# Kernel optimization log

Hardware: AMD Instinct MI355X
Metric: run time of the kernel (lower is better)

## Reference

```python
import jax, jax.numpy as jnp
import numpy as np
import math

NUM_POSE_FEAT = 64  # -> pos emb dim 128
N_NBR = 16
TEMP = 10000.0


def pos2posemb2d(pos, num_pos_feats=NUM_POSE_FEAT):
    # PETR-style 2D sine embedding; pos: (..., 2) in [0,1)
    scale = 2.0 * math.pi
    pos = pos * scale
    dim_t = jnp.arange(num_pos_feats, dtype=pos.dtype)
    dim_t = TEMP ** (2.0 * jnp.floor(dim_t / 2.0) / num_pos_feats)
    pos_x = pos[..., 0:1] / dim_t  # (..., P)
    pos_y = pos[..., 1:2] / dim_t

    def interleave(p):
        return jnp.stack([jnp.sin(p[..., 0::2]), jnp.cos(p[..., 1::2])], axis=-1).reshape(p.shape[:-1] + (-1,))

    return jnp.concatenate([interleave(pos_y), interleave(pos_x)], axis=-1)  # (..., 2P)


def mlp(x, W1, b1, W2, b2):
    return jax.nn.relu(x @ W1 + b1) @ W2 + b2


def setup_inputs() -> dict:
    key = jax.random.key(0)
    ks = jax.random.split(key, 12)
    B, S, L, D, P2 = 4, 4096, 8192, 256, 2 * NUM_POSE_FEAT
    s1 = 1.0 / np.sqrt(P2)
    s2 = 1.0 / np.sqrt(D)
    return {
        "memory": jax.random.normal(ks[0], (B, L, D), jnp.float32),
        "mem_coor": jax.random.uniform(ks[1], (B, L, 2), dtype=jnp.float32),
        "q_coor": jax.random.uniform(ks[2], (B, S, 2), dtype=jnp.float32),
        "Wq1": jax.random.normal(ks[3], (P2, D), jnp.float32) * s1,
        "bq1": jnp.zeros((D,), jnp.float32),
        "Wq2": jax.random.normal(ks[4], (D, D), jnp.float32) * s2,
        "bq2": jnp.zeros((D,), jnp.float32),
        "Wk1": jax.random.normal(ks[5], (P2, D), jnp.float32) * s1,
        "bk1": jnp.zeros((D,), jnp.float32),
        "Wk2": jax.random.normal(ks[6], (D, D), jnp.float32) * s2,
        "bk2": jnp.zeros((D,), jnp.float32),
        "B": 4,
    }


def reference(memory, mem_coor, q_coor, Wq1, bq1, Wq2, bq2, Wk1, bk1, Wk2, bk2, B):
    # memory: (B, L, D); mem_coor: (B, L, 2); q_coor: (B, S, 2)
    Bn, L, D = memory.shape
    query = mlp(pos2posemb2d(q_coor), Wq1, bq1, Wq2, bq2)      # (B, S, D) query = query_pos
    mem_pos = mlp(pos2posemb2d(mem_coor), Wk1, bk1, Wk2, bk2)  # (B, L, D)
    kv_pe = mem_pos + memory                                   # (B, L, D)

    # squared pairwise distances via matmul expansion (monotonic in true distance,
    # only the top-k ORDER is consumed downstream)
    q2 = jnp.sum(q_coor * q_coor, axis=-1)                     # (B, S)
    m2 = jnp.sum(mem_coor * mem_coor, axis=-1)                 # (B, L)
    d2 = q2[:, :, None] + m2[:, None, :] - 2.0 * jnp.einsum("bsc,blc->bsl", q_coor, mem_coor)
    _, idx = jax.lax.top_k(-d2, N_NBR)                         # (B, S, k) nearest-neighbor indices

    bidx = jnp.arange(Bn)[:, None, None]
    kv_m = kv_pe[bidx, idx]                                    # (B, S, k, D) gathered pos-embedded memory
    prod = query[:, :, None, :] * kv_m / jnp.sqrt(jnp.asarray(D, query.dtype))
    attn = jax.nn.softmax(prod, axis=-1)                       # softmax over feature dim D
    out = attn * memory[bidx, idx]                             # (B, S, k, D)
    return out
```

## Files before the change

kernel.cpp:

```cpp
#include <hip/hip_runtime.h>
#include <math.h>

#define NB 4
#define NS 4096
#define NL 8192
#define ND 256
#define NP2 128
#define NK 16

#define GCELLS 32
#define GH 0.03125f
#define CAP 256
#define EPSM 2e-5f

__device__ __forceinline__ float sum_sq_np(float x, float y) {
#pragma clang fp contract(off)
  return x * x + y * y;
}

__device__ __forceinline__ float dist2_fast(float q2, float m2, float qx, float qy,
                                            float mx, float my) {
#pragma clang fp contract(off)
  float dot = __builtin_fmaf(qy, my, qx * mx);
  float s = q2 + m2;
  return __builtin_fmaf(-2.0f, dot, s);
}

__device__ __forceinline__ unsigned f32ord(float f) {
  unsigned u = __float_as_uint(f);
  return u ^ ((unsigned)((int)u >> 31) | 0x80000000u);
}

template <int NR>
__device__ __forceinline__ unsigned extract16(const unsigned long long* candrow,
                                              int cnt, int lane,
                                              int* __restrict__ outp) {
  unsigned long long myc[NR];
#pragma unroll
  for (int j = 0; j < NR; ++j) {
    int p = lane + j * 64;
    myc[j] = (p < cnt) ? candrow[p] : ~0ull;
  }
  unsigned tau_ord = 0xffffffffu;
#pragma unroll 1
  for (int r = 0; r < NK; ++r) {
    unsigned long long m = myc[0];
#pragma unroll
    for (int j = 1; j < NR; ++j) m = myc[j] < m ? myc[j] : m;
#pragma unroll
    for (int o = 1; o < 64; o <<= 1) {
      unsigned long long other = __shfl_xor(m, o, 64);
      if (other < m) m = other;
    }
    if (lane == 0) outp[r] = (int)(unsigned)(m & 0xffffffffull);
    if (r == NK - 1) tau_ord = (unsigned)(m >> 32);
#pragma unroll
    for (int j = 0; j < NR; ++j)
      if (myc[j] == m) myc[j] = ~0ull;
  }
  return tau_ord;
}

#define RPAD 20
#define NSBLK (NB * NS / 16)

struct __align__(16) MlpSmem {
  union {
    float pe[NP2][RPAD];
    float h[ND][RPAD];
  };
};

__device__ __forceinline__ void fma16(float* acc, float wt, const float4& p0,
                                      const float4& p1, const float4& p2,
                                      const float4& p3) {
  acc[0] = fmaf(p0.x, wt, acc[0]);   acc[1] = fmaf(p0.y, wt, acc[1]);
  acc[2] = fmaf(p0.z, wt, acc[2]);   acc[3] = fmaf(p0.w, wt, acc[3]);
  acc[4] = fmaf(p1.x, wt, acc[4]);   acc[5] = fmaf(p1.y, wt, acc[5]);
  acc[6] = fmaf(p1.z, wt, acc[6]);   acc[7] = fmaf(p1.w, wt, acc[7]);
  acc[8] = fmaf(p2.x, wt, acc[8]);   acc[9] = fmaf(p2.y, wt, acc[9]);
  acc[10] = fmaf(p2.z, wt, acc[10]); acc[11] = fmaf(p2.w, wt, acc[11]);
  acc[12] = fmaf(p3.x, wt, acc[12]); acc[13] = fmaf(p3.y, wt, acc[13]);
  acc[14] = fmaf(p3.z, wt, acc[14]); acc[15] = fmaf(p3.w, wt, acc[15]);
}

__device__ __forceinline__ void loadW8(const float* __restrict__ W, int k0,
                                       int tid, float* w0, float* w1) {
#pragma unroll
  for (int u = 0; u < 8; ++u) {
    w0[u] = W[(size_t)(k0 + u) * ND + tid];
    w1[u] = W[(size_t)(k0 + u) * ND + 128 + tid];
  }
}

__device__ __forceinline__ void consume8(const float (*L)[RPAD], int k0,
                                         const float* w0, const float* w1,
                                         float* acc0, float* acc1) {
#pragma unroll
  for (int u = 0; u < 8; ++u) {
    int k = k0 + u;
    float4 p0 = *(const float4*)&L[k][0];
    float4 p1 = *(const float4*)&L[k][4];
    float4 p2 = *(const float4*)&L[k][8];
    float4 p3 = *(const float4*)&L[k][12];
    fma16(acc0, w0[u], p0, p1, p2, p3);
    fma16(acc1, w1[u], p0, p1, p2, p3);
  }
}

__global__ __launch_bounds__(128) void mlp_fused_kernel(
    const float* __restrict__ q_coor, const float* __restrict__ mem_coor,
    const float* __restrict__ memory,
    const float* __restrict__ Wq1, const float* __restrict__ bq1,
    const float* __restrict__ Wq2, const float* __restrict__ bq2,
    const float* __restrict__ Wk1, const float* __restrict__ bk1,
    const float* __restrict__ Wk2, const float* __restrict__ bk2,
    float* __restrict__ query, float* __restrict__ kv_pe) {
  __shared__ MlpSmem sm;
  const int tid = threadIdx.x;
  const int bid = blockIdx.x;
  const bool isS = bid < NSBLK;
  const float* coor = isS ? q_coor : mem_coor;
  const float* W1 = isS ? Wq1 : Wk1;
  const float* b1 = isS ? bq1 : bk1;
  const float* W2 = isS ? Wq2 : Wk2;
  const float* b2 = isS ? bq2 : bk2;
  const float* addmem = isS ? (const float*)nullptr : memory;
  float* out = isS ? query : kv_pe;
  const int row0 = (isS ? bid : bid - NSBLK) * 16;

#pragma unroll
  for (int it = 0; it < 8; ++it) {
    int e = tid + it * 128;
    int r = e >> 6;
    int rem = e & 63;
    int part = rem >> 5;
    int j = rem & 31;
    float c = coor[(size_t)(row0 + r) * 2 + (part ^ 1)];
    float inv_t = exp2f((float)j * -0.4152410118609718f);
    float arg = c * 6.2831853071795864f * inv_t;
    float sv, cv;
    sincosf(arg, &sv, &cv);
    int k0 = part * 64 + 2 * j;
    sm.pe[k0][r] = sv;
    sm.pe[k0 + 1][r] = cv;
  }
  __syncthreads();

  float acc0[16], acc1[16];
  float wA0[8], wA1[8], wB0[8], wB1[8];
  {
    float bb0 = b1[tid], bb1 = b1[tid + 128];
#pragma unroll
    for (int r = 0; r < 16; ++r) { acc0[r] = bb0; acc1[r] = bb1; }
  }
  loadW8(W1, 0, tid, wA0, wA1);
#pragma unroll 1
  for (int k0 = 0; k0 < NP2; k0 += 16) {
    loadW8(W1, k0 + 8, tid, wB0, wB1);
    consume8(sm.pe, k0, wA0, wA1, acc0, acc1);
    if (k0 + 16 < NP2) loadW8(W1, k0 + 16, tid, wA0, wA1);
    consume8(sm.pe, k0 + 8, wB0, wB1, acc0, acc1);
  }
  __syncthreads();
#pragma unroll
  for (int r = 0; r < 16; ++r) {
    sm.h[tid][r] = fmaxf(acc0[r], 0.0f);
    sm.h[tid + 128][r] = fmaxf(acc1[r], 0.0f);
  }
  __syncthreads();

  {
    float bb0 = b2[tid], bb1 = b2[tid + 128];
#pragma unroll
    for (int r = 0; r < 16; ++r) { acc0[r] = bb0; acc1[r] = bb1; }
  }
  loadW8(W2, 0, tid, wA0, wA1);
#pragma unroll 1
  for (int k0 = 0; k0 < ND; k0 += 16) {
    loadW8(W2, k0 + 8, tid, wB0, wB1);
    consume8(sm.h, k0, wA0, wA1, acc0, acc1);
    if (k0 + 16 < ND) loadW8(W2, k0 + 16, tid, wA0, wA1);
    consume8(sm.h, k0 + 8, wB0, wB1, acc0, acc1);
  }
#pragma unroll
  for (int r = 0; r < 16; ++r) {
    size_t g = (size_t)(row0 + r);
    float v0 = acc0[r], v1 = acc1[r];
    if (addmem) {
      v0 += addmem[g * ND + tid];
      v1 += addmem[g * ND + 128 + tid];
    }
    out[g * ND + tid] = v0;
    out[g * ND + 128 + tid] = v1;
  }
}

__global__ __launch_bounds__(1024) void build_kernel(
    const float* __restrict__ mem_coor, const float* __restrict__ q_coor,
    float4* __restrict__ sorted, int* __restrict__ starts,
    int* __restrict__ qord) {
  __shared__ int hist[GCELLS * GCELLS];
  __shared__ int cur[GCELLS * GCELLS];
  const int bid = blockIdx.x;
  const bool isMem = bid < NB;
  const int b = isMem ? bid : bid - NB;
  const int n = isMem ? NL : NS;
  const float2* cc = (const float2*)(isMem ? mem_coor : q_coor) + (size_t)b * n;
  const int tid = threadIdx.x;

  hist[tid] = 0;
  __syncthreads();
  for (int it = 0; it < n / 1024; ++it) {
    float2 c = cc[it * 1024 + tid];
    int cx = (int)(c.x * 32.0f); cx = cx > 31 ? 31 : cx;
    int cy = (int)(c.y * 32.0f); cy = cy > 31 ? 31 : cy;
    atomicAdd(&hist[cy * GCELLS + cx], 1);
  }
  __syncthreads();
  const int own = hist[tid];
  for (int o = 1; o < 1024; o <<= 1) {
    int v = (tid >= o) ? hist[tid - o] : 0;
    __syncthreads();
    hist[tid] += v;
    __syncthreads();
  }
  const int excl = hist[tid] - own;
  if (isMem) {
    starts[b * (GCELLS * GCELLS + 1) + tid] = excl;
    if (tid == 0) starts[b * (GCELLS * GCELLS + 1) + GCELLS * GCELLS] = NL;
  }
  cur[tid] = excl;
  __syncthreads();
  for (int it = 0; it < n / 1024; ++it) {
    int i = it * 1024 + tid;
    float2 c = cc[i];
    int cx = (int)(c.x * 32.0f); cx = cx > 31 ? 31 : cx;
    int cy = (int)(c.y * 32.0f); cy = cy > 31 ? 31 : cy;
    int pos = atomicAdd(&cur[cy * GCELLS + cx], 1);
    if (isMem) {
      sorted[(size_t)b * NL + pos] =
          make_float4(c.x, c.y, sum_sq_np(c.x, c.y), __int_as_float(i));
    } else {
      qord[b * NS + pos] = i;
    }
  }
}

__global__ __launch_bounds__(256) void topk_kernel(
    const float* __restrict__ q_coor, const float4* __restrict__ sorted,
    const int* __restrict__ starts, int* __restrict__ idx_out) {
  __shared__ unsigned long long cand[4][CAP];
  __shared__ int fcnt[4];

  const int tid = threadIdx.x;
  const int wv = tid >> 6;
  const int lane = tid & 63;
  const int qi = blockIdx.x * 4 + wv;
  const int b = qi >> 12;

  const float qx = q_coor[(size_t)qi * 2 + 0];
  const float qy = q_coor[(size_t)qi * 2 + 1];
  const float q2 = sum_sq_np(qx, qy);
  const float4* sp = sorted + (size_t)b * NL;
  const int* st = starts + b * (GCELLS * GCELLS + 1);
  int* outp = idx_out + (size_t)qi * NK;

  int ci = (int)(qx * 32.0f); ci = ci > 31 ? 31 : ci;
  int cj = (int)(qy * 32.0f); cj = cj > 31 ? 31 : cj;

  int x0 = ci - 1 < 0 ? 0 : ci - 1, x1 = ci + 1 > 31 ? 31 : ci + 1;
  int y0 = cj - 1 < 0 ? 0 : cj - 1, y1 = cj + 1 > 31 ? 31 : cj + 1;
  int cnt = 0;
  bool ovf = false;

  auto span = [&](int y, int xa, int xb) {
    int s0 = st[y * GCELLS + xa];
    int e0 = st[y * GCELLS + xb + 1];
    int len = e0 - s0;
    if (cnt + len > CAP) { ovf = true; return; }
    for (int i = lane; i < len; i += 64) {
      float4 rx = sp[s0 + i];
      float d2 = dist2_fast(q2, rx.z, qx, qy, rx.x, rx.y);
      cand[wv][cnt + i] = ((unsigned long long)f32ord(d2) << 32) |
                          (unsigned)__float_as_int(rx.w);
    }
    cnt += len;
  };

  for (int y = y0; y <= y1 && !ovf; ++y) span(y, x0, x1);

  int R = 1;
  while (!ovf) {
    unsigned tau_ord;
    if (cnt <= 128) tau_ord = extract16<2>(cand[wv], cnt, lane, outp);
    else            tau_ord = extract16<4>(cand[wv], cnt, lane, outp);
    float dxl = x0 > 0  ? qx - (float)x0 * GH        : 1e30f;
    float dxr = x1 < 31 ? (float)(x1 + 1) * GH - qx  : 1e30f;
    float dyl = y0 > 0  ? qy - (float)y0 * GH        : 1e30f;
    float dyr = y1 < 31 ? (float)(y1 + 1) * GH - qy  : 1e30f;
    float dmin = fminf(fminf(dxl, dxr), fminf(dyl, dyr));
    float bound = dmin * dmin - EPSM;
    if (cnt >= NK && tau_ord < f32ord(bound)) return;
    if (x0 == 0 && x1 == 31 && y0 == 0 && y1 == 31) return;
    ++R;
    int nx0 = ci - R < 0 ? 0 : ci - R, nx1 = ci + R > 31 ? 31 : ci + R;
    int ny0 = cj - R < 0 ? 0 : cj - R, ny1 = cj + R > 31 ? 31 : cj + R;
    if (ny0 < y0) span(ny0, nx0, nx1);
    if (ny1 > y1 && !ovf) span(ny1, nx0, nx1);
    for (int y = y0; y <= y1 && !ovf; ++y) {
      if (nx0 < x0) span(y, nx0, x0 - 1);
      if (nx1 > x1 && !ovf) span(y, x1 + 1, nx1);
    }
    x0 = nx0; x1 = nx1; y0 = ny0; y1 = ny1;
  }

  float lmin = __builtin_inff();
#pragma unroll 8
  for (int it = 0; it < NL / 64; ++it) {
    float4 rx = sp[it * 64 + lane];
    float d2 = dist2_fast(q2, rx.z, qx, qy, rx.x, rx.y);
    lmin = fminf(lmin, d2);
  }
  float tau;
  {
    float curm = lmin;
    for (int r = 0; r < NK; ++r) {
      float m = curm;
#pragma unroll
      for (int o = 1; o < 64; o <<= 1) m = fminf(m, __shfl_xor(m, o, 64));
      tau = m;
      if (curm == m) curm = __builtin_inff();
    }
  }
  if (lane == 0) fcnt[wv] = 0;
#pragma unroll 4
  for (int it = 0; it < NL / 64; ++it) {
    float4 rx = sp[it * 64 + lane];
    float d2 = dist2_fast(q2, rx.z, qx, qy, rx.x, rx.y);
    bool hit = (d2 <= tau);
    unsigned long long mask = __ballot(hit);
    if (mask) {
      int base = fcnt[wv];
      if (hit) {
        int pos = base + (int)__popcll(mask & ((1ull << lane) - 1ull));
        if (pos < CAP) {
          cand[wv][pos] = ((unsigned long long)f32ord(d2) << 32) |
                          (unsigned)__float_as_int(rx.w);
        }
      }
      if (lane == 0) fcnt[wv] = base + (int)__popcll(mask);
    }
  }
  int N = fcnt[wv];
  if (N > CAP) N = CAP;
  extract16<4>(cand[wv], N, lane, outp);
}

__global__ __launch_bounds__(256) void attn_kernel(
    const float* __restrict__ query, const float* __restrict__ kv_pe,
    const float* __restrict__ memory, const int* __restrict__ idx,
    const int* __restrict__ qord, float* __restrict__ out) {
  const int tid = threadIdx.x;
  const int wv = tid >> 6;
  const int lane = tid & 63;
  const int bid = ((blockIdx.x & 7) * (NB * NS / 4 / 8)) + (blockIdx.x >> 3);
  const int qpos = bid * 4 + wv;
  const int b = qpos >> 12;
  const int qi = b * NS + qord[qpos];

  float4 q4 = *(const float4*)(query + (size_t)qi * ND + lane * 4);
  int lv = 0;
  if (lane < NK) lv = idx[(size_t)qi * NK + lane];

#pragma unroll 4
  for (int k = 0; k < NK; ++k) {
    int l = __shfl(lv, k, 64);
    size_t base = ((size_t)b * NL + l) * ND + (size_t)lane * 4;
    float4 kv = *(const float4*)(kv_pe + base);
    float4 mm = *(const float4*)(memory + base);
    float p0 = q4.x * kv.x * 0.0625f;
    float p1 = q4.y * kv.y * 0.0625f;
    float p2 = q4.z * kv.z * 0.0625f;
    float p3 = q4.w * kv.w * 0.0625f;
    float mx = fmaxf(fmaxf(p0, p1), fmaxf(p2, p3));
#pragma unroll
    for (int o = 1; o < 64; o <<= 1) mx = fmaxf(mx, __shfl_xor(mx, o, 64));
    float e0 = expf(p0 - mx);
    float e1 = expf(p1 - mx);
    float e2 = expf(p2 - mx);
    float e3 = expf(p3 - mx);
    float s = (e0 + e1) + (e2 + e3);
#pragma unroll
    for (int o = 1; o < 64; o <<= 1) s += __shfl_xor(s, o, 64);
    float inv = 1.0f / s;
    float4 o4;
    o4.x = e0 * inv * mm.x;
    o4.y = e1 * inv * mm.y;
    o4.z = e2 * inv * mm.z;
    o4.w = e3 * inv * mm.w;
    *(float4*)(out + ((size_t)qi * NK + k) * ND + (size_t)lane * 4) = o4;
  }
}

extern "C" void kernel_launch(void* const* d_in, const int* in_sizes, int n_in,
                              void* d_out, int out_size, void* d_ws, size_t ws_size,
                              hipStream_t stream) {
  (void)in_sizes; (void)n_in; (void)out_size; (void)ws_size;
  const float* memory   = (const float*)d_in[0];
  const float* mem_coor = (const float*)d_in[1];
  const float* q_coor   = (const float*)d_in[2];
  const float* Wq1 = (const float*)d_in[3];
  const float* bq1 = (const float*)d_in[4];
  const float* Wq2 = (const float*)d_in[5];
  const float* bq2 = (const float*)d_in[6];
  const float* Wk1 = (const float*)d_in[7];
  const float* bk1 = (const float*)d_in[8];
  const float* Wk2 = (const float*)d_in[9];
  const float* bk2 = (const float*)d_in[10];

  float* query = (float*)d_ws;
  float* kv_pe = query + (size_t)NB * NS * ND;
  int*   nidx  = (int*)(kv_pe + (size_t)NB * NL * ND);
  int*   qord  = nidx + (size_t)NB * NS * NK;
  float* outp  = (float*)d_out;

  float4* sorted  = (float4*)d_out;
  int*    gstarts = (int*)((char*)d_out + (size_t)NB * NL * 16);

  hipLaunchKernelGGL(build_kernel, dim3(2 * NB), dim3(1024), 0, stream,
                     mem_coor, q_coor, sorted, gstarts, qord);
  hipLaunchKernelGGL(mlp_fused_kernel, dim3(NSBLK + NB * NL / 16), dim3(128),
                     0, stream, q_coor, mem_coor, memory,
                     Wq1, bq1, Wq2, bq2, Wk1, bk1, Wk2, bk2, query, kv_pe);
  hipLaunchKernelGGL(topk_kernel, dim3(NB * NS / 4), dim3(256), 0, stream,
                     q_coor, sorted, gstarts, nidx);
  hipLaunchKernelGGL(attn_kernel, dim3(NB * NS / 4), dim3(256), 0, stream,
                     query, kv_pe, memory, nidx, qord, outp);
}
```

Baseline: 541.8 us.

## Fuse MLP and top-k kernels into one interleaved horizontal launch

Merges the independent MLP positional-embedding kernel and the grid-based top-k neighbor search into a single launch. Blocks are interleaved in groups of 11 (3 MLP blocks, 8 top-k blocks), so compute-heavy MLP work and latency-bound search run concurrently on the CUs. Top-k blocks shrink from 4 to 2 waves to match the 128-thread block size, and shared memory becomes a union of both layouts. The cost is that occupancy and register use are now set by whichever path is heavier, which can reduce occupancy for the lighter path.

```diff
diff --git a/kernel.cpp b/kernel.cpp
--- a/kernel.cpp
+++ b/kernel.cpp
@@ -63,11 +63,25 @@
 
 #define RPAD 20
 #define NSBLK (NB * NS / 16)
+#define NMLPBLK (NSBLK + NB * NL / 16)
+#define NTKBLK (NB * NS / 2)
 
 struct __align__(16) MlpSmem {
   union {
     float pe[NP2][RPAD];
     float h[ND][RPAD];
+  };
+};
+
+struct __align__(16) TopkSmem {
+  unsigned long long cand[2][CAP];
+  int fcnt[2];
+};
+
+struct __align__(16) FusedSmem {
+  union {
+    MlpSmem mlp;
+    TopkSmem tk;
   };
 };
 
@@ -108,7 +122,8 @@
   }
 }
 
-__global__ __launch_bounds__(128) void mlp_fused_kernel(
+__device__ __forceinline__ void mlp_block(
+    int bid, int tid, MlpSmem& sm,
     const float* __restrict__ q_coor, const float* __restrict__ mem_coor,
     const float* __restrict__ memory,
     const float* __restrict__ Wq1, const float* __restrict__ bq1,
@@ -116,9 +131,6 @@
     const float* __restrict__ Wk1, const float* __restrict__ bk1,
     const float* __restrict__ Wk2, const float* __restrict__ bk2,
     float* __restrict__ query, float* __restrict__ kv_pe) {
-  __shared__ MlpSmem sm;
-  const int tid = threadIdx.x;
-  const int bid = blockIdx.x;
   const bool isS = bid < NSBLK;
   const float* coor = isS ? q_coor : mem_coor;
   const float* W1 = isS ? Wq1 : Wk1;
@@ -196,67 +208,13 @@
   }
 }
 
-__global__ __launch_bounds__(1024) void build_kernel(
-    const float* __restrict__ mem_coor, const float* __restrict__ q_coor,
-    float4* __restrict__ sorted, int* __restrict__ starts,
-    int* __restrict__ qord) {
-  __shared__ int hist[GCELLS * GCELLS];
-  __shared__ int cur[GCELLS * GCELLS];
-  const int bid = blockIdx.x;
-  const bool isMem = bid < NB;
-  const int b = isMem ? bid : bid - NB;
-  const int n = isMem ? NL : NS;
-  const float2* cc = (const float2*)(isMem ? mem_coor : q_coor) + (size_t)b * n;
-  const int tid = threadIdx.x;
-
-  hist[tid] = 0;
-  __syncthreads();
-  for (int it = 0; it < n / 1024; ++it) {
-    float2 c = cc[it * 1024 + tid];
-    int cx = (int)(c.x * 32.0f); cx = cx > 31 ? 31 : cx;
-    int cy = (int)(c.y * 32.0f); cy = cy > 31 ? 31 : cy;
-    atomicAdd(&hist[cy * GCELLS + cx], 1);
-  }
-  __syncthreads();
-  const int own = hist[tid];
-  for (int o = 1; o < 1024; o <<= 1) {
-    int v = (tid >= o) ? hist[tid - o] : 0;
-    __syncthreads();
-    hist[tid] += v;
-    __syncthreads();
-  }
-  const int excl = hist[tid] - own;
-  if (isMem) {
-    starts[b * (GCELLS * GCELLS + 1) + tid] = excl;
-    if (tid == 0) starts[b * (GCELLS * GCELLS + 1) + GCELLS * GCELLS] = NL;
-  }
-  cur[tid] = excl;
-  __syncthreads();
-  for (int it = 0; it < n / 1024; ++it) {
-    int i = it * 1024 + tid;
-    float2 c = cc[i];
-    int cx = (int)(c.x * 32.0f); cx = cx > 31 ? 31 : cx;
-    int cy = (int)(c.y * 32.0f); cy = cy > 31 ? 31 : cy;
-    int pos = atomicAdd(&cur[cy * GCELLS + cx], 1);
-    if (isMem) {
-      sorted[(size_t)b * NL + pos] =
-          make_float4(c.x, c.y, sum_sq_np(c.x, c.y), __int_as_float(i));
-    } else {
-      qord[b * NS + pos] = i;
-    }
-  }
-}
-
-__global__ __launch_bounds__(256) void topk_kernel(
+__device__ __forceinline__ void topk_block(
+    int tbid, int tid, TopkSmem& sm,
     const float* __restrict__ q_coor, const float4* __restrict__ sorted,
     const int* __restrict__ starts, int* __restrict__ idx_out) {
-  __shared__ unsigned long long cand[4][CAP];
-  __shared__ int fcnt[4];
-
-  const int tid = threadIdx.x;
   const int wv = tid >> 6;
   const int lane = tid & 63;
-  const int qi = blockIdx.x * 4 + wv;
+  const int qi = tbid * 2 + wv;
   const int b = qi >> 12;
 
   const float qx = q_coor[(size_t)qi * 2 + 0];
@@ -265,6 +223,7 @@
   const float4* sp = sorted + (size_t)b * NL;
   const int* st = starts + b * (GCELLS * GCELLS + 1);
   int* outp = idx_out + (size_t)qi * NK;
+  unsigned long long* crow = sm.cand[wv];
 
   int ci = (int)(qx * 32.0f); ci = ci > 31 ? 31 : ci;
   int cj = (int)(qy * 32.0f); cj = cj > 31 ? 31 : cj;
@@ -282,8 +241,8 @@
     for (int i = lane; i < len; i += 64) {
       float4 rx = sp[s0 + i];
       float d2 = dist2_fast(q2, rx.z, qx, qy, rx.x, rx.y);
-      cand[wv][cnt + i] = ((unsigned long long)f32ord(d2) << 32) |
-                          (unsigned)__float_as_int(rx.w);
+      crow[cnt + i] = ((unsigned long long)f32ord(d2) << 32) |
+                      (unsigned)__float_as_int(rx.w);
     }
     cnt += len;
   };
@@ -293,8 +252,8 @@
   int R = 1;
   while (!ovf) {
     unsigned tau_ord;
-    if (cnt <= 128) tau_ord = extract16<2>(cand[wv], cnt, lane, outp);
-    else            tau_ord = extract16<4>(cand[wv], cnt, lane, outp);
+    if (cnt <= 128) tau_ord = extract16<2>(crow, cnt, lane, outp);
+    else            tau_ord = extract16<4>(crow, cnt, lane, outp);
     float dxl = x0 > 0  ? qx - (float)x0 * GH        : 1e30f;
     float dxr = x1 < 31 ? (float)(x1 + 1) * GH - qx  : 1e30f;
     float dyl = y0 > 0  ? qy - (float)y0 * GH        : 1e30f;
@@ -333,7 +292,7 @@
       if (curm == m) curm = __builtin_inff();
     }
   }
-  if (lane == 0) fcnt[wv] = 0;
+  if (lane == 0) sm.fcnt[wv] = 0;
 #pragma unroll 4
   for (int it = 0; it < NL / 64; ++it) {
     float4 rx = sp[it * 64 + lane];
@@ -341,20 +300,95 @@
     bool hit = (d2 <= tau);
     unsigned long long mask = __ballot(hit);
     if (mask) {
-      int base = fcnt[wv];
+      int base = sm.fcnt[wv];
       if (hit) {
         int pos = base + (int)__popcll(mask & ((1ull << lane) - 1ull));
         if (pos < CAP) {
-          cand[wv][pos] = ((unsigned long long)f32ord(d2) << 32) |
-                          (unsigned)__float_as_int(rx.w);
+          crow[pos] = ((unsigned long long)f32ord(d2) << 32) |
+                      (unsigned)__float_as_int(rx.w);
         }
       }
-      if (lane == 0) fcnt[wv] = base + (int)__popcll(mask);
-    }
-  }
-  int N = fcnt[wv];
+      if (lane == 0) sm.fcnt[wv] = base + (int)__popcll(mask);
+    }
+  }
+  int N = sm.fcnt[wv];
   if (N > CAP) N = CAP;
-  extract16<4>(cand[wv], N, lane, outp);
+  extract16<4>(crow, N, lane, outp);
+}
+
+__global__ __launch_bounds__(128) void fused_mlp_topk_kernel(
+    const float* __restrict__ q_coor, const float* __restrict__ mem_coor,
+    const float* __restrict__ memory,
+    const float* __restrict__ Wq1, const float* __restrict__ bq1,
+    const float* __restrict__ Wq2, const float* __restrict__ bq2,
+    const float* __restrict__ Wk1, const float* __restrict__ bk1,
+    const float* __restrict__ Wk2, const float* __restrict__ bk2,
+    float* __restrict__ query, float* __restrict__ kv_pe,
+    const float4* __restrict__ sorted, const int* __restrict__ starts,
+    int* __restrict__ idx_out) {
+  __shared__ FusedSmem sm;
+  const int g = blockIdx.x;
+  const int grp = g / 11;
+  const int rem = g - grp * 11;
+  const int tid = threadIdx.x;
+  if (rem < 3) {
+    mlp_block(grp * 3 + rem, tid, sm.mlp, q_coor, mem_coor, memory,
+              Wq1, bq1, Wq2, bq2, Wk1, bk1, Wk2, bk2, query, kv_pe);
+  } else {
+    topk_block(grp * 8 + (rem - 3), tid, sm.tk, q_coor, sorted, starts,
+               idx_out);
+  }
+}
+
+__global__ __launch_bounds__(1024) void build_kernel(
+    const float* __restrict__ mem_coor, const float* __restrict__ q_coor,
+    float4* __restrict__ sorted, int* __restrict__ starts,
+    int* __restrict__ qord) {
+  __shared__ int hist[GCELLS * GCELLS];
+  __shared__ int cur[GCELLS * GCELLS];
+  const int bid = blockIdx.x;
+  const bool isMem = bid < NB;
+  const int b = isMem ? bid : bid - NB;
+  const int n = isMem ? NL : NS;
+  const float2* cc = (const float2*)(isMem ? mem_coor : q_coor) + (size_t)b * n;
+  const int tid = threadIdx.x;
+
+  hist[tid] = 0;
+  __syncthreads();
+  for (int it = 0; it < n / 1024; ++it) {
+    float2 c = cc[it * 1024 + tid];
+    int cx = (int)(c.x * 32.0f); cx = cx > 31 ? 31 : cx;
+    int cy = (int)(c.y * 32.0f); cy = cy > 31 ? 31 : cy;
+    atomicAdd(&hist[cy * GCELLS + cx], 1);
+  }
+  __syncthreads();
+  const int own = hist[tid];
+  for (int o = 1; o < 1024; o <<= 1) {
+    int v = (tid >= o) ? hist[tid - o] : 0;
+    __syncthreads();
+    hist[tid] += v;
+    __syncthreads();
+  }
+  const int excl = hist[tid] - own;
+  if (isMem) {
+    starts[b * (GCELLS * GCELLS + 1) + tid] = excl;
+    if (tid == 0) starts[b * (GCELLS * GCELLS + 1) + GCELLS * GCELLS] = NL;
+  }
+  cur[tid] = excl;
+  __syncthreads();
+  for (int it = 0; it < n / 1024; ++it) {
+    int i = it * 1024 + tid;
+    float2 c = cc[i];
+    int cx = (int)(c.x * 32.0f); cx = cx > 31 ? 31 : cx;
+    int cy = (int)(c.y * 32.0f); cy = cy > 31 ? 31 : cy;
+    int pos = atomicAdd(&cur[cy * GCELLS + cx], 1);
+    if (isMem) {
+      sorted[(size_t)b * NL + pos] =
+          make_float4(c.x, c.y, sum_sq_np(c.x, c.y), __int_as_float(i));
+    } else {
+      qord[b * NS + pos] = i;
+    }
+  }
 }
 
 __global__ __launch_bounds__(256) void attn_kernel(
@@ -430,11 +464,10 @@
 
   hipLaunchKernelGGL(build_kernel, dim3(2 * NB), dim3(1024), 0, stream,
                      mem_coor, q_coor, sorted, gstarts, qord);
-  hipLaunchKernelGGL(mlp_fused_kernel, dim3(NSBLK + NB * NL / 16), dim3(128),
+  hipLaunchKernelGGL(fused_mlp_topk_kernel, dim3(11 * 1024), dim3(128),
                      0, stream, q_coor, mem_coor, memory,
-                     Wq1, bq1, Wq2, bq2, Wk1, bk1, Wk2, bk2, query, kv_pe);
-  hipLaunchKernelGGL(topk_kernel, dim3(NB * NS / 4), dim3(256), 0, stream,
-                     q_coor, sorted, gstarts, nidx);
+                     Wq1, bq1, Wq2, bq2, Wk1, bk1, Wk2, bk2, query, kv_pe,
+                     sorted, gstarts, nidx);
   hipLaunchKernelGGL(attn_kernel, dim3(NB * NS / 4), dim3(256), 0, stream,
                      query, kv_pe, memory, nidx, qord, outp);
 }
```

New measurement: 580.5 us. 7.1% more time.
